# Kernel tuning notes

Hardware: AMD Instinct MI355X
Metric: run time of the kernel (lower is better)

The kernel has to match this reference:

```python
import jax, jax.numpy as jnp
import numpy as np
import math

B, T, S = 32, 64, 128
D = 768          # d_model / embed_dim / output_dim
E2 = 1024        # enc_hid_dim * 2
H = 512          # dec_hid_dim
V = 50257        # vocab
I = E2 + D       # GRU input size


def setup_inputs() -> dict:
    key = jax.random.key(0)
    ks = jax.random.split(key, 14)
    s = 0.02
    return {
        "input_ids": jax.random.randint(ks[0], (B, T), 0, V),
        "attention_mask": jnp.ones((B, T), dtype=jnp.int64),
        "enc_hidden": jax.random.normal(ks[1], (B, H), jnp.float32),
        "enc_outputs": jax.random.normal(ks[2], (B, S, E2), jnp.float32),
        "embed_W": jax.random.normal(ks[3], (V, D), jnp.float32) * s,
        "attn_W": jax.random.normal(ks[4], (E2 + H, H), jnp.float32) * s,  # input order: (dec_hidden, enc_out)
        "attn_b": jnp.zeros((H,), jnp.float32),
        "val_w": jax.random.normal(ks[5], (H, 1), jnp.float32) * s,
        "W_ih": jax.random.normal(ks[6], (3 * H, I), jnp.float32) * s,
        "W_hh": jax.random.normal(ks[7], (3 * H, H), jnp.float32) * s,
        "b_ih": jnp.zeros((3 * H,), jnp.float32),
        "b_hh": jnp.zeros((3 * H,), jnp.float32),
        "fc_W": jax.random.normal(ks[8], (D, E2 + H + D), jnp.float32) * s,  # torch Linear weight [out,in]
        "fc_b": jnp.zeros((D,), jnp.float32),
    }


def _decode_loop(input_ids, attention_mask, enc_hidden, enc_outputs,
                 embed_W, attn_W, attn_b, val_w, W_ih, W_hh, b_ih, b_hh, fc_W, fc_b):
    # eval mode (dropout off), teacher_forcing_ratio = 1.0 -> input at step t is input_ids[:, t]
    ids = input_ids * attention_mask
    scale = jnp.asarray(math.sqrt(embed_W.shape[1]), embed_W.dtype)
    # cat order in Attention is (dec_hidden_repeated, encoder_outputs)
    Wa_h = attn_W[:H]          # [H, H]
    Wa_e = attn_W[H:]          # [E2, H]
    enc_proj = jnp.einsum('bse,eh->bsh', enc_outputs, Wa_e) + attn_b  # [B,S,H] precomputed

    def step(h, ids_t):
        emb = embed_W[ids_t] * scale                                  # [B,D]
        energy = jnp.tanh(enc_proj + (h @ Wa_h)[:, None, :])          # [B,S,H]
        attn = jax.nn.softmax((energy @ val_w)[..., 0], axis=1)       # [B,S]
        weighted = jnp.einsum('bs,bse->be', attn, enc_outputs)        # [B,E2]
        x = jnp.concatenate([emb, weighted], axis=1)                  # [B,I]
        gi = x @ W_ih.T + b_ih                                        # [B,3H]
        gh = h @ W_hh.T + b_hh
        i_r, i_z, i_n = jnp.split(gi, 3, axis=1)
        h_r, h_z, h_n = jnp.split(gh, 3, axis=1)
        r = jax.nn.sigmoid(i_r + h_r)
        z = jax.nn.sigmoid(i_z + h_z)
        n = jnp.tanh(i_n + r * h_n)
        h_new = (1.0 - z) * n + z * h                                 # [B,H]
        pred = jnp.concatenate([h_new, weighted, emb], axis=1) @ fc_W.T + fc_b  # [B,D]
        return h_new, pred

    _, preds = jax.lax.scan(step, enc_hidden, ids.T)                  # preds [T,B,D]
    return jnp.transpose(preds, (1, 0, 2))                            # [B,T,D]


def reference(input_ids, attention_mask, enc_hidden, enc_outputs,
              embed_W, attn_W, attn_b, val_w, W_ih, W_hh, b_ih, b_hh, fc_W, fc_b):
    return _decode_loop(input_ids, attention_mask, enc_hidden, enc_outputs,
                        embed_W, attn_W, attn_b, val_w, W_ih, W_hh, b_ih, b_hh, fc_W, fc_b)
```

## Files before the change

kernel.cpp:

```cpp
#include <hip/hip_runtime.h>


constexpr int BB  = 32;
constexpr int TT  = 64;
constexpr int SS  = 128;
constexpr int DD  = 768;
constexpr int EE  = 1024;
constexpr int HH  = 512;
constexpr int G3  = 1536;
constexpr int II  = 1792;
constexpr int CIN = 2304;
constexpr int NBLK = 256;

typedef _Float16 half2_t __attribute__((ext_vector_type(2)));
typedef _Float16 half8_t __attribute__((ext_vector_type(8)));
typedef float f32x4_t __attribute__((ext_vector_type(4)));

__device__ __forceinline__ float fast_rcp(float x) { return __builtin_amdgcn_rcpf(x); }
__device__ __forceinline__ float tanh_f(float x) {
  float e = __expf(2.f * x);
  return 1.f - 2.f * fast_rcp(1.f + e);
}
__device__ __forceinline__ float sigmoid_f(float x) { return fast_rcp(1.f + __expf(-x)); }
__device__ __forceinline__ unsigned packh2(float x, float y) {
  half2_t h; h[0] = (_Float16)x; h[1] = (_Float16)y;
  return __builtin_bit_cast(unsigned, h);
}
__device__ __forceinline__ float h2lo(unsigned v) {
  return (float)__builtin_bit_cast(half2_t, v)[0];
}
__device__ __forceinline__ float h2hi(unsigned v) {
  return (float)__builtin_bit_cast(half2_t, v)[1];
}
__device__ __forceinline__ unsigned short f2h(float f) {
  _Float16 h = (_Float16)f; return __builtin_bit_cast(unsigned short, h);
}
__device__ __forceinline__ float u16tof(unsigned short u) {
  return (float)__builtin_bit_cast(_Float16, u);
}
__device__ __forceinline__ float fdot2(unsigned a, unsigned b, float c) {
#if __has_builtin(__builtin_amdgcn_fdot2)
  return __builtin_amdgcn_fdot2(__builtin_bit_cast(half2_t, a),
                                __builtin_bit_cast(half2_t, b), c, false);
#else
  half2_t ha = __builtin_bit_cast(half2_t, a);
  half2_t hb = __builtin_bit_cast(half2_t, b);
  return fmaf((float)ha[1], (float)hb[1], fmaf((float)ha[0], (float)hb[0], c));
#endif
}

__device__ __forceinline__ unsigned long long ald64(const unsigned long long* p) {
  return __hip_atomic_load(p, __ATOMIC_RELAXED, __HIP_MEMORY_SCOPE_AGENT);
}
__device__ __forceinline__ void ast64(unsigned long long* p, unsigned long long v) {
  __hip_atomic_store(p, v, __ATOMIC_RELAXED, __HIP_MEMORY_SCOPE_AGENT);
}
__device__ __forceinline__ unsigned long long mkchunk(unsigned pair, unsigned seq) {
  return (unsigned long long)pair | ((unsigned long long)seq << 32);
}

constexpr int PB0 = 33;
constexpr int PB1 = PB0 + 2048;
constexpr int PB2 = PB1 + 2048;
constexpr int PB3 = PB2 + 384;
constexpr int PB4 = PB3 + 864;
constexpr int PB5 = PB4 + 1536;
constexpr int PB6 = PB5 + 1536;
constexpr int PB7 = PB6 + 256;
constexpr int PB8 = PB7 + 512;

__device__ __forceinline__ void cast8(const float* __restrict__ in,
                                      unsigned short* __restrict__ out,
                                      int blk, int tid) {
  int i = (blk * 256 + tid) * 8;
  float4 a = *(const float4*)(in + i);
  float4 b = *(const float4*)(in + i + 4);
  unsigned short r[8] = {f2h(a.x), f2h(a.y), f2h(a.z), f2h(a.w),
                         f2h(b.x), f2h(b.y), f2h(b.z), f2h(b.w)};
  *(uint4*)(out + i) = *(uint4*)r;
}
__device__ __forceinline__ void pack_row(const float* __restrict__ src, int srcld,
                                         unsigned short* __restrict__ dst, int W,
                                         int r, int tid) {
  const float* s = src + (size_t)r * srcld;
  unsigned short* d = dst + (size_t)r * W;
  for (int c = tid * 4; c < W; c += 256 * 4) {
    float4 v = *(const float4*)(s + c);
    unsigned short q[4] = {f2h(v.x), f2h(v.y), f2h(v.z), f2h(v.w)};
    *(unsigned long long*)(d + c) = *(unsigned long long*)q;
  }
}
__device__ __forceinline__ void tcast_tile(const float* __restrict__ in, int R,
                                           int C, unsigned short* __restrict__ out,
                                           int bx, int by, int tid, float (*t)[33]) {
  const int c0 = bx * 32, r0 = by * 32;
  const int tx = tid & 31, ty = tid >> 5;
  for (int dy = 0; dy < 32; dy += 8)
    t[ty + dy][tx] = in[(size_t)(r0 + ty + dy) * C + c0 + tx];
  __syncthreads();
  for (int dy = 0; dy < 32; dy += 8)
    out[(size_t)(c0 + ty + dy) * R + r0 + tx] = f2h(t[tx][ty + dy]);
}

__global__ __launch_bounds__(256) void prep_kernel(
    const int* __restrict__ ids, const float* __restrict__ embed_W,
    const float* __restrict__ enc_hidden, const float* __restrict__ enc_outputs,
    const float* __restrict__ attn_W, const float* __restrict__ W_ih,
    const float* __restrict__ W_hh, const float* __restrict__ fc_W,
    unsigned short* __restrict__ Xh, unsigned short* __restrict__ enc_h,
    unsigned short* __restrict__ whh_h, unsigned short* __restrict__ fcw_h,
    unsigned short* __restrict__ wih768, unsigned short* __restrict__ wihw_h,
    unsigned short* __restrict__ wa_t, unsigned short* __restrict__ waet,
    unsigned long long* __restrict__ hx, unsigned long long* __restrict__ ps)
{
  __shared__ float tbuf[32][33];
  const int bidx = blockIdx.x;
  const int tid = threadIdx.x;
  if (bidx < PB0) {
    int b = bidx;
    if (b < BB) {
      unsigned pair = packh2(enc_hidden[(size_t)b * HH + 2 * tid],
                             enc_hidden[(size_t)b * HH + 2 * tid + 1]);
      hx[(size_t)b * 256 + tid] = mkchunk(pair, 0u);
    } else {
      for (int i = tid; i < BB * 8 * 64; i += 256) ps[i] = 0ull;
    }
  } else if (bidx < PB1) {
    int row = bidx - PB0;
    int id = ids[row];
    const float scale = 27.712812921102035f;
    const float* src = embed_W + (size_t)id * DD;
    unsigned short* dst = Xh + (size_t)row * CIN + (HH + EE);
    for (int c = tid; c < DD; c += 256) dst[c] = f2h(src[c] * scale);
  } else if (bidx < PB2) {
    cast8(enc_outputs, enc_h, bidx - PB1, tid);
  } else if (bidx < PB3) {
    cast8(W_hh, whh_h, bidx - PB2, tid);
  } else if (bidx < PB4) {
    cast8(fc_W, fcw_h, bidx - PB3, tid);
  } else if (bidx < PB5) {
    pack_row(W_ih, II, wih768, DD, bidx - PB4, tid);
  } else if (bidx < PB6) {
    pack_row(W_ih + DD, II, wihw_h, EE, bidx - PB5, tid);
  } else if (bidx < PB7) {
    int q = bidx - PB6;
    tcast_tile(attn_W, HH, HH, wa_t, q & 15, q >> 4, tid, tbuf);
  } else {
    int q = bidx - PB7;
    tcast_tile(attn_W + (size_t)HH * HH, EE, HH, waet, q & 15, q >> 4, tid, tbuf);
  }
}

template <bool F32OUT>
__device__ __forceinline__ void mfma_tile128(
    const unsigned short* __restrict__ Ah, int lda,
    const unsigned short* __restrict__ Bh, int ldb,
    const float* __restrict__ bias,
    unsigned short* __restrict__ Ch, float* __restrict__ Cf, int ldc, int K,
    int m0, int n0)
{
  const int lane = threadIdx.x & 63;
  const int wv = threadIdx.x >> 6;
  const int wr = wv >> 1, wc = wv & 1;
  const int rbase = m0 + wr * 64 + (lane & 15);
  const int cbase = n0 + wc * 64 + (lane & 15);
  const int koff = (lane >> 4) * 8;
  f32x4_t acc[4][4] = {};
  for (int k0 = 0; k0 < K; k0 += 32) {
    half8_t a[4], b[4];
#pragma unroll
    for (int i = 0; i < 4; ++i) {
      a[i] = *(const half8_t*)(Ah + (size_t)(rbase + i * 16) * lda + k0 + koff);
      b[i] = *(const half8_t*)(Bh + (size_t)(cbase + i * 16) * ldb + k0 + koff);
    }
#pragma unroll
    for (int mf = 0; mf < 4; ++mf)
#pragma unroll
      for (int nf = 0; nf < 4; ++nf)
        acc[mf][nf] =
            __builtin_amdgcn_mfma_f32_16x16x32_f16(a[mf], b[nf], acc[mf][nf], 0, 0, 0);
  }
#pragma unroll
  for (int mf = 0; mf < 4; ++mf)
#pragma unroll
    for (int nf = 0; nf < 4; ++nf) {
      const int col = n0 + wc * 64 + nf * 16 + (lane & 15);
      const float bv = bias ? bias[col] : 0.f;
#pragma unroll
      for (int r = 0; r < 4; ++r) {
        const int rr = m0 + wr * 64 + mf * 16 + (lane >> 4) * 4 + r;
        if (F32OUT) Cf[(size_t)rr * ldc + col] = acc[mf][nf][r] + bv;
        else        Ch[(size_t)rr * ldc + col] = f2h(acc[mf][nf][r] + bv);
      }
    }
}

__global__ __launch_bounds__(256) void gemm3_kernel(
    const unsigned short* __restrict__ enc_h,
    const unsigned short* __restrict__ waet,
    const float* __restrict__ attn_b,
    unsigned short* __restrict__ ep_h,
    const unsigned short* __restrict__ Xh,
    const unsigned short* __restrict__ wih768,
    const float* __restrict__ b_ih,
    unsigned short* __restrict__ geh,
    const unsigned short* __restrict__ wihw_h,
    unsigned short* __restrict__ encW)
{
  const int id = blockIdx.x;
  if (id < 128) {
    int nt = id & 3, mt = id >> 2;
    mfma_tile128<false>(enc_h, EE, waet, EE, attn_b, ep_h, nullptr, HH, EE,
                        mt * 128, nt * 128);
  } else if (id < 320) {
    int q = id - 128, nt = q % 12, mt = q / 12;
    mfma_tile128<false>(Xh + (HH + EE), CIN, wih768, DD, b_ih, geh, nullptr,
                        G3, DD, mt * 128, nt * 128);
  } else {
    int q = id - 320, nt = q % 12, mt = q / 12;
    mfma_tile128<false>(enc_h, EE, wihw_h, EE, nullptr, encW, nullptr,
                        G3, EE, mt * 128, nt * 128);
  }
}

__global__ __launch_bounds__(256) void out_gemm_kernel(
    const unsigned short* __restrict__ Xh,
    const unsigned short* __restrict__ fcw_h,
    const float* __restrict__ fc_b, float* __restrict__ out)
{
  mfma_tile128<true>(Xh, CIN, fcw_h, CIN, fc_b, nullptr, out, DD, CIN,
                     blockIdx.y * 128, blockIdx.x * 128);
}

__global__ __launch_bounds__(512, 1) void recur_kernel(
    const unsigned short* __restrict__ wa_t,
    const unsigned short* __restrict__ whh_h,
    const float* __restrict__ val_w,
    const float* __restrict__ b_hh,
    const unsigned* __restrict__ ep32,
    const unsigned* __restrict__ enc32,
    const unsigned short* __restrict__ encW,
    const unsigned short* __restrict__ geh,
    const float* __restrict__ enc_hidden,
    unsigned long long* __restrict__ hx,
    unsigned long long* __restrict__ ps,
    unsigned short* __restrict__ Xh)
{
  __shared__ unsigned s_encw[3][64][64];
  __shared__ unsigned s_ep[SS][33];
  __shared__ unsigned s_enc[SS][64];
  __shared__ unsigned s_h2[256];
  __shared__ float s_p[4][8][64];
  __shared__ unsigned s_hwa2[32];
  __shared__ unsigned s_vw2[32];
  __shared__ float s_scp[SS];
  __shared__ unsigned s_ps[8][64];
  __shared__ float s_sc[SS];
  __shared__ float s_part[4][128];
  __shared__ unsigned s_at2[64];

  const int tid = threadIdx.x;
  const int b = blockIdx.x & 31;
  const int g = blockIdx.x >> 5;
  const int jj = tid & 63, sub = tid >> 6;
  const int jglob = g * 64 + jj;

  for (int idx = tid; idx < 3 * 64 * 64; idx += 512) {
    int gt = idx >> 12, j2 = (idx >> 6) & 63, sp = idx & 63;
    int col = gt * HH + g * 64 + j2;
    unsigned lo = encW[((size_t)b * SS + 2 * sp) * G3 + col];
    unsigned hi = encW[((size_t)b * SS + 2 * sp + 1) * G3 + col];
    s_encw[gt][j2][sp ^ (j2 & 31)] = lo | (hi << 16);
  }
  for (int idx = tid; idx < SS * 32; idx += 512) {
    int s = idx >> 5, p = idx & 31;
    s_ep[s][p] = ep32[((size_t)b * SS + s) * 256 + g * 32 + p];
  }
  for (int idx = tid; idx < SS * 64; idx += 512) {
    int s = idx >> 6, p = idx & 63;
    s_enc[s][p] = enc32[((size_t)b * SS + s) * 512 + g * 64 + p];
  }
  if (tid < 32)
    s_vw2[tid] = packh2(val_w[g * 64 + 2 * tid], val_w[g * 64 + 2 * tid + 1]);
  float bhh0 = 0.f, bhh1 = 0.f, bhh2 = 0.f, hprev = 0.f;
  if (tid < 64) {
    bhh0 = b_hh[g * 64 + tid];
    bhh1 = b_hh[HH + g * 64 + tid];
    bhh2 = b_hh[2 * HH + g * 64 + tid];
    hprev = enc_hidden[(size_t)b * HH + g * 64 + tid];
  }
  __syncthreads();

  unsigned long long* hxb = hx + (size_t)b * 256;
  unsigned long long* psb = ps + (size_t)b * 512;

  for (unsigned t = 0; t < TT; ++t) {
    if (tid < 256) {
      unsigned long long v;
      for (;;) {
        v = ald64(hxb + tid);
        if ((unsigned)(v >> 32) == t) break;
        __builtin_amdgcn_s_sleep(1);
      }
      s_h2[tid] = (unsigned)v;
    }
    __syncthreads();
    {
      const unsigned* wa = (const unsigned*)(wa_t + (size_t)jglob * HH) + sub * 32;
      const unsigned* w0 = (const unsigned*)(whh_h + (size_t)jglob * HH) + sub * 32;
      const unsigned* w1 = (const unsigned*)(whh_h + (size_t)(HH + jglob) * HH) + sub * 32;
      const unsigned* w2 = (const unsigned*)(whh_h + (size_t)(2 * HH + jglob) * HH) + sub * 32;
      float a0 = 0.f, a1 = 0.f, a2 = 0.f, a3 = 0.f;
#pragma unroll
      for (int it = 0; it < 8; ++it) {
        uint4 hp = *(const uint4*)(s_h2 + sub * 32 + 4 * it);
        uint4 va = *(const uint4*)(wa + 4 * it);
        uint4 v0 = *(const uint4*)(w0 + 4 * it);
        uint4 v1 = *(const uint4*)(w1 + 4 * it);
        uint4 v2 = *(const uint4*)(w2 + 4 * it);
        a0 = fdot2(hp.x, va.x, a0); a0 = fdot2(hp.y, va.y, a0);
        a0 = fdot2(hp.z, va.z, a0); a0 = fdot2(hp.w, va.w, a0);
        a1 = fdot2(hp.x, v0.x, a1); a1 = fdot2(hp.y, v0.y, a1);
        a1 = fdot2(hp.z, v0.z, a1); a1 = fdot2(hp.w, v0.w, a1);
        a2 = fdot2(hp.x, v1.x, a2); a2 = fdot2(hp.y, v1.y, a2);
        a2 = fdot2(hp.z, v1.z, a2); a2 = fdot2(hp.w, v1.w, a2);
        a3 = fdot2(hp.x, v2.x, a3); a3 = fdot2(hp.y, v2.y, a3);
        a3 = fdot2(hp.z, v2.z, a3); a3 = fdot2(hp.w, v2.w, a3);
      }
      s_p[0][sub][jj] = a0;
      s_p[1][sub][jj] = a1;
      s_p[2][sub][jj] = a2;
      s_p[3][sub][jj] = a3;
    }
    __syncthreads();
    float ghr = 0.f, ghz = 0.f, ghn = 0.f;
    if (tid < 64) {
      float hw = 0.f;
#pragma unroll
      for (int s8 = 0; s8 < 8; ++s8) {
        hw  += s_p[0][s8][tid];
        ghr += s_p[1][s8][tid];
        ghz += s_p[2][s8][tid];
        ghn += s_p[3][s8][tid];
      }
      ghr += bhh0; ghz += bhh1; ghn += bhh2;
      float o = __shfl_xor(hw, 1);
      if (!(tid & 1)) s_hwa2[tid >> 1] = packh2(hw, o);
    }
    __syncthreads();
    {
      const int s_ = tid >> 2, q = tid & 3;
      float a0 = 0.f;
#pragma unroll
      for (int p = 0; p < 8; ++p) {
        unsigned v  = s_ep[s_][q * 8 + p];
        unsigned hh = s_hwa2[q * 8 + p];
        unsigned vv = s_vw2[q * 8 + p];
        a0 = fmaf(tanh_f(h2lo(v) + h2lo(hh)), h2lo(vv), a0);
        a0 = fmaf(tanh_f(h2hi(v) + h2hi(hh)), h2hi(vv), a0);
      }
      a0 += __shfl_xor(a0, 1);
      a0 += __shfl_xor(a0, 2);
      if (q == 0) s_scp[s_] = a0;
    }
    __syncthreads();
    if (tid < 64)
      ast64(psb + g * 64 + tid,
            mkchunk(packh2(s_scp[2 * tid], s_scp[2 * tid + 1]), t + 1));

    {
      const int pg = tid >> 6, pc = tid & 63;
      unsigned long long v;
      for (;;) {
        v = ald64(psb + pg * 64 + pc);
        if ((unsigned)(v >> 32) == t + 1) break;
        __builtin_amdgcn_s_sleep(1);
      }
      s_ps[pg][pc] = (unsigned)v;
    }
    __syncthreads();
    if (tid < 64) {
      float v0 = 0.f, v1 = 0.f;
#pragma unroll
      for (int gg = 0; gg < 8; ++gg) {
        unsigned p = s_ps[gg][tid];
        v0 += h2lo(p);
        v1 += h2hi(p);
      }
      float m = fmaxf(v0, v1);
#pragma unroll
      for (int mm = 32; mm >= 1; mm >>= 1) m = fmaxf(m, __shfl_xor(m, mm));
      float e0 = __expf(v0 - m), e1 = __expf(v1 - m);
      float sum = e0 + e1;
#pragma unroll
      for (int mm = 32; mm >= 1; mm >>= 1) sum += __shfl_xor(sum, mm);
      float rs = fast_rcp(sum);
      e0 *= rs; e1 *= rs;
      s_sc[2 * tid] = e0;
      s_sc[2 * tid + 1] = e1;
      s_at2[tid] = packh2(e0, e1);
    }
    __syncthreads();
    if (tid >= 256) {
      const int qs = (tid - 256) >> 6, ep2 = tid & 63;
      float w0 = 0.f, w1 = 0.f;
#pragma unroll 8
      for (int s = 0; s < 32; ++s) {
        unsigned v = s_enc[qs * 32 + s][ep2];
        float a = s_sc[qs * 32 + s];
        w0 = fmaf(a, h2lo(v), w0);
        w1 = fmaf(a, h2hi(v), w1);
      }
      s_part[qs][2 * ep2]     = w0;
      s_part[qs][2 * ep2 + 1] = w1;
    }
    __syncthreads();
    if (tid < 64) {
      float a0 = 0.f, a1 = 0.f, a2 = 0.f;
#pragma unroll 8
      for (int sp = 0; sp < 64; ++sp) {
        unsigned at = s_at2[sp];
        const int sx = sp ^ (tid & 31);
        a0 = fdot2(at, s_encw[0][tid][sx], a0);
        a1 = fdot2(at, s_encw[1][tid][sx], a1);
        a2 = fdot2(at, s_encw[2][tid][sx], a2);
      }
      const unsigned short* geb = geh + (size_t)(b * TT + t) * G3 + jglob;
      float r = sigmoid_f(a0 + u16tof(geb[0]) + ghr);
      float z = sigmoid_f(a1 + u16tof(geb[HH]) + ghz);
      float nn = tanh_f(a2 + u16tof(geb[2 * HH]) + r * ghn);
      float hnew = (1.f - z) * nn + z * hprev;
      hprev = hnew;
      Xh[(size_t)(b * TT + t) * CIN + jglob] = f2h(hnew);
      float o = __shfl_xor(hnew, 1);
      if (!(tid & 1))
        ast64(hxb + g * 32 + (tid >> 1), mkchunk(packh2(hnew, o), t + 1));
    } else if (tid >= 128 && tid < 256) {
      const int e = tid - 128;
      float w = s_part[0][e] + s_part[1][e] + s_part[2][e] + s_part[3][e];
      Xh[(size_t)(b * TT + t) * CIN + HH + g * 128 + e] = f2h(w);
    }
    __syncthreads();
  }
}

extern "C" void kernel_launch(void* const* d_in, const int* in_sizes, int n_in,
                              void* d_out, int out_size, void* d_ws, size_t ws_size,
                              hipStream_t stream) {
  (void)in_sizes; (void)n_in; (void)out_size; (void)ws_size;
  const int* input_ids = (const int*)d_in[0];
  const float* enc_hidden  = (const float*)d_in[2];
  const float* enc_outputs = (const float*)d_in[3];
  const float* embed_W = (const float*)d_in[4];
  const float* attn_W  = (const float*)d_in[5];
  const float* attn_b  = (const float*)d_in[6];
  const float* val_w   = (const float*)d_in[7];
  const float* W_ih    = (const float*)d_in[8];
  const float* W_hh    = (const float*)d_in[9];
  const float* b_ih    = (const float*)d_in[10];
  const float* b_hh    = (const float*)d_in[11];
  const float* fc_W    = (const float*)d_in[12];
  const float* fc_b    = (const float*)d_in[13];
  float* out = (float*)d_out;

  char* wsb = (char*)d_ws;
  unsigned short* Xh      = (unsigned short*)wsb; wsb += (size_t)BB*TT*CIN*2;
  unsigned short* geh     = (unsigned short*)wsb; wsb += (size_t)BB*TT*G3*2;
  unsigned short* enc_h   = (unsigned short*)wsb; wsb += (size_t)BB*SS*EE*2;
  unsigned short* ep_h    = (unsigned short*)wsb; wsb += (size_t)BB*SS*HH*2;
  unsigned short* wihw_h  = (unsigned short*)wsb; wsb += (size_t)G3*EE*2;
  unsigned short* encW    = (unsigned short*)wsb; wsb += (size_t)BB*SS*G3*2;
  unsigned short* whh_h   = (unsigned short*)wsb; wsb += (size_t)G3*HH*2;
  unsigned short* wa_t    = (unsigned short*)wsb; wsb += (size_t)HH*HH*2;
  unsigned short* waet    = (unsigned short*)wsb; wsb += (size_t)HH*EE*2;
  unsigned short* wih768  = (unsigned short*)wsb; wsb += (size_t)G3*DD*2;
  unsigned short* fcw_h   = (unsigned short*)wsb; wsb += (size_t)DD*CIN*2;
  unsigned long long* hx  = (unsigned long long*)wsb; wsb += (size_t)BB*256*8;
  unsigned long long* ps  = (unsigned long long*)wsb; wsb += (size_t)BB*512*8;

  prep_kernel<<<PB8, 256, 0, stream>>>(
      input_ids, embed_W, enc_hidden, enc_outputs, attn_W, W_ih, W_hh, fc_W,
      Xh, enc_h, whh_h, fcw_h, wih768, wihw_h, wa_t, waet, hx, ps);

  gemm3_kernel<<<704, 256, 0, stream>>>(
      enc_h, waet, attn_b, ep_h, Xh, wih768, b_ih, geh, wihw_h, encW);

  void* args[] = {
      (void*)&wa_t, (void*)&whh_h, (void*)&val_w, (void*)&b_hh,
      (void*)&ep_h, (void*)&enc_h, (void*)&encW, (void*)&geh, (void*)&enc_hidden,
      (void*)&hx, (void*)&ps, (void*)&Xh};
  hipLaunchCooperativeKernel((void*)recur_kernel, dim3(NBLK), dim3(512),
                             args, 0, stream);

  out_gemm_kernel<<<dim3(DD / 128, (BB * TT) / 128), 256, 0, stream>>>(
      Xh, fcw_h, fc_b, out);
}
```

Measured before the change: 619.9 us.

## Cut per-step barriers in recurrence and double-buffer MFMA GEMM loads

Each wave now polls its own 32 hidden-state pairs and broadcasts them with lane shuffles instead of staging them in shared memory behind a block barrier. The attention score partials are published straight from the reducing lanes, which removes another barrier and a shared buffer. The context-vector accumulation now runs in the same phase as the GRU gate update, which shortens the critical path of each time step. Separately, the MFMA tile loop prefetches the next K slice into registers before computing the current one, trading extra registers for hidden load latency.

```diff
diff --git a/kernel.cpp b/kernel.cpp
--- a/kernel.cpp
+++ b/kernel.cpp
@@ -166,12 +166,18 @@
   const int cbase = n0 + wc * 64 + (lane & 15);
   const int koff = (lane >> 4) * 8;
   f32x4_t acc[4][4] = {};
-  for (int k0 = 0; k0 < K; k0 += 32) {
-    half8_t a[4], b[4];
+  half8_t a[4], b[4];
+#pragma unroll
+  for (int i = 0; i < 4; ++i) {
+    a[i] = *(const half8_t*)(Ah + (size_t)(rbase + i * 16) * lda + koff);
+    b[i] = *(const half8_t*)(Bh + (size_t)(cbase + i * 16) * ldb + koff);
+  }
+  for (int k0 = 32; k0 < K; k0 += 32) {
+    half8_t an[4], bn[4];
 #pragma unroll
     for (int i = 0; i < 4; ++i) {
-      a[i] = *(const half8_t*)(Ah + (size_t)(rbase + i * 16) * lda + k0 + koff);
-      b[i] = *(const half8_t*)(Bh + (size_t)(cbase + i * 16) * ldb + k0 + koff);
+      an[i] = *(const half8_t*)(Ah + (size_t)(rbase + i * 16) * lda + k0 + koff);
+      bn[i] = *(const half8_t*)(Bh + (size_t)(cbase + i * 16) * ldb + k0 + koff);
     }
 #pragma unroll
     for (int mf = 0; mf < 4; ++mf)
@@ -179,7 +185,15 @@
       for (int nf = 0; nf < 4; ++nf)
         acc[mf][nf] =
             __builtin_amdgcn_mfma_f32_16x16x32_f16(a[mf], b[nf], acc[mf][nf], 0, 0, 0);
-  }
+#pragma unroll
+    for (int i = 0; i < 4; ++i) { a[i] = an[i]; b[i] = bn[i]; }
+  }
+#pragma unroll
+  for (int mf = 0; mf < 4; ++mf)
+#pragma unroll
+    for (int nf = 0; nf < 4; ++nf)
+      acc[mf][nf] =
+          __builtin_amdgcn_mfma_f32_16x16x32_f16(a[mf], b[nf], acc[mf][nf], 0, 0, 0);
 #pragma unroll
   for (int mf = 0; mf < 4; ++mf)
 #pragma unroll
@@ -249,11 +263,9 @@
   __shared__ unsigned s_encw[3][64][64];
   __shared__ unsigned s_ep[SS][33];
   __shared__ unsigned s_enc[SS][64];
-  __shared__ unsigned s_h2[256];
   __shared__ float s_p[4][8][64];
   __shared__ unsigned s_hwa2[32];
   __shared__ unsigned s_vw2[32];
-  __shared__ float s_scp[SS];
   __shared__ unsigned s_ps[8][64];
   __shared__ float s_sc[SS];
   __shared__ float s_part[4][128];
@@ -262,8 +274,9 @@
   const int tid = threadIdx.x;
   const int b = blockIdx.x & 31;
   const int g = blockIdx.x >> 5;
-  const int jj = tid & 63, sub = tid >> 6;
-  const int jglob = g * 64 + jj;
+  const int lane = tid & 63;
+  const int wv = tid >> 6;
+  const int jglob = g * 64 + lane;
 
   for (int idx = tid; idx < 3 * 64 * 64; idx += 512) {
     int gt = idx >> 12, j2 = (idx >> 6) & 63, sp = idx & 63;
@@ -294,43 +307,48 @@
   unsigned long long* hxb = hx + (size_t)b * 256;
   unsigned long long* psb = ps + (size_t)b * 512;
 
+  const unsigned* wa = (const unsigned*)(wa_t + (size_t)jglob * HH) + wv * 32;
+  const unsigned* w0 = (const unsigned*)(whh_h + (size_t)jglob * HH) + wv * 32;
+  const unsigned* w1 = (const unsigned*)(whh_h + (size_t)(HH + jglob) * HH) + wv * 32;
+  const unsigned* w2 = (const unsigned*)(whh_h + (size_t)(2 * HH + jglob) * HH) + wv * 32;
+
   for (unsigned t = 0; t < TT; ++t) {
-    if (tid < 256) {
+    unsigned hpair;
+    {
+      const unsigned long long* src = hxb + wv * 32 + (lane & 31);
       unsigned long long v;
       for (;;) {
-        v = ald64(hxb + tid);
-        if ((unsigned)(v >> 32) == t) break;
+        v = ald64(src);
+        if (__all((unsigned)(v >> 32) == t)) break;
         __builtin_amdgcn_s_sleep(1);
       }
-      s_h2[tid] = (unsigned)v;
-    }
-    __syncthreads();
+      hpair = (unsigned)v;
+    }
     {
-      const unsigned* wa = (const unsigned*)(wa_t + (size_t)jglob * HH) + sub * 32;
-      const unsigned* w0 = (const unsigned*)(whh_h + (size_t)jglob * HH) + sub * 32;
-      const unsigned* w1 = (const unsigned*)(whh_h + (size_t)(HH + jglob) * HH) + sub * 32;
-      const unsigned* w2 = (const unsigned*)(whh_h + (size_t)(2 * HH + jglob) * HH) + sub * 32;
       float a0 = 0.f, a1 = 0.f, a2 = 0.f, a3 = 0.f;
 #pragma unroll
-      for (int it = 0; it < 8; ++it) {
-        uint4 hp = *(const uint4*)(s_h2 + sub * 32 + 4 * it);
-        uint4 va = *(const uint4*)(wa + 4 * it);
-        uint4 v0 = *(const uint4*)(w0 + 4 * it);
-        uint4 v1 = *(const uint4*)(w1 + 4 * it);
-        uint4 v2 = *(const uint4*)(w2 + 4 * it);
-        a0 = fdot2(hp.x, va.x, a0); a0 = fdot2(hp.y, va.y, a0);
-        a0 = fdot2(hp.z, va.z, a0); a0 = fdot2(hp.w, va.w, a0);
-        a1 = fdot2(hp.x, v0.x, a1); a1 = fdot2(hp.y, v0.y, a1);
-        a1 = fdot2(hp.z, v0.z, a1); a1 = fdot2(hp.w, v0.w, a1);
-        a2 = fdot2(hp.x, v1.x, a2); a2 = fdot2(hp.y, v1.y, a2);
-        a2 = fdot2(hp.z, v1.z, a2); a2 = fdot2(hp.w, v1.w, a2);
-        a3 = fdot2(hp.x, v2.x, a3); a3 = fdot2(hp.y, v2.y, a3);
-        a3 = fdot2(hp.z, v2.z, a3); a3 = fdot2(hp.w, v2.w, a3);
-      }
-      s_p[0][sub][jj] = a0;
-      s_p[1][sub][jj] = a1;
-      s_p[2][sub][jj] = a2;
-      s_p[3][sub][jj] = a3;
+      for (int p4 = 0; p4 < 8; ++p4) {
+        uint4 va = *(const uint4*)(wa + 4 * p4);
+        uint4 v0 = *(const uint4*)(w0 + 4 * p4);
+        uint4 v1 = *(const uint4*)(w1 + 4 * p4);
+        uint4 v2 = *(const uint4*)(w2 + 4 * p4);
+        unsigned h0 = __shfl(hpair, 4 * p4 + 0);
+        unsigned h1 = __shfl(hpair, 4 * p4 + 1);
+        unsigned h2 = __shfl(hpair, 4 * p4 + 2);
+        unsigned h3 = __shfl(hpair, 4 * p4 + 3);
+        a0 = fdot2(h0, va.x, a0); a0 = fdot2(h1, va.y, a0);
+        a0 = fdot2(h2, va.z, a0); a0 = fdot2(h3, va.w, a0);
+        a1 = fdot2(h0, v0.x, a1); a1 = fdot2(h1, v0.y, a1);
+        a1 = fdot2(h2, v0.z, a1); a1 = fdot2(h3, v0.w, a1);
+        a2 = fdot2(h0, v1.x, a2); a2 = fdot2(h1, v1.y, a2);
+        a2 = fdot2(h2, v1.z, a2); a2 = fdot2(h3, v1.w, a2);
+        a3 = fdot2(h0, v2.x, a3); a3 = fdot2(h1, v2.y, a3);
+        a3 = fdot2(h2, v2.z, a3); a3 = fdot2(h3, v2.w, a3);
+      }
+      s_p[0][wv][lane] = a0;
+      s_p[1][wv][lane] = a1;
+      s_p[2][wv][lane] = a2;
+      s_p[3][wv][lane] = a3;
     }
     __syncthreads();
     float ghr = 0.f, ghz = 0.f, ghn = 0.f;
@@ -361,12 +379,10 @@
       }
       a0 += __shfl_xor(a0, 1);
       a0 += __shfl_xor(a0, 2);
-      if (q == 0) s_scp[s_] = a0;
-    }
-    __syncthreads();
-    if (tid < 64)
-      ast64(psb + g * 64 + tid,
-            mkchunk(packh2(s_scp[2 * tid], s_scp[2 * tid + 1]), t + 1));
+      float nb = __shfl_down(a0, 4);
+      if ((tid & 7) == 0)
+        ast64(psb + g * 64 + (s_ >> 1), mkchunk(packh2(a0, nb), t + 1));
+    }
 
     {
       const int pg = tid >> 6, pc = tid & 63;
@@ -399,20 +415,6 @@
       s_sc[2 * tid] = e0;
       s_sc[2 * tid + 1] = e1;
       s_at2[tid] = packh2(e0, e1);
-    }
-    __syncthreads();
-    if (tid >= 256) {
-      const int qs = (tid - 256) >> 6, ep2 = tid & 63;
-      float w0 = 0.f, w1 = 0.f;
-#pragma unroll 8
-      for (int s = 0; s < 32; ++s) {
-        unsigned v = s_enc[qs * 32 + s][ep2];
-        float a = s_sc[qs * 32 + s];
-        w0 = fmaf(a, h2lo(v), w0);
-        w1 = fmaf(a, h2hi(v), w1);
-      }
-      s_part[qs][2 * ep2]     = w0;
-      s_part[qs][2 * ep2 + 1] = w1;
     }
     __syncthreads();
     if (tid < 64) {
@@ -435,12 +437,25 @@
       float o = __shfl_xor(hnew, 1);
       if (!(tid & 1))
         ast64(hxb + g * 32 + (tid >> 1), mkchunk(packh2(hnew, o), t + 1));
-    } else if (tid >= 128 && tid < 256) {
+    } else if (tid >= 256) {
+      const int qs = (tid - 256) >> 6, ep2 = tid & 63;
+      float w0 = 0.f, w1 = 0.f;
+#pragma unroll 8
+      for (int s = 0; s < 32; ++s) {
+        unsigned v = s_enc[qs * 32 + s][ep2];
+        float a = s_sc[qs * 32 + s];
+        w0 = fmaf(a, h2lo(v), w0);
+        w1 = fmaf(a, h2hi(v), w1);
+      }
+      s_part[qs][2 * ep2]     = w0;
+      s_part[qs][2 * ep2 + 1] = w1;
+    }
+    __syncthreads();
+    if (tid >= 128 && tid < 256) {
       const int e = tid - 128;
       float w = s_part[0][e] + s_part[1][e] + s_part[2][e] + s_part[3][e];
       Xh[(size_t)(b * TT + t) * CIN + HH + g * 128 + e] = f2h(w);
     }
-    __syncthreads();
   }
 }
 
```

Result: faster. 592.1 us (median of 2 runs) (-4.5%).
